# Kernel optimization log

Hardware: AMD Instinct MI355X
Metric: run time of the kernel (lower is better)

## Reference

```python
import jax, jax.numpy as jnp
import numpy as np

S = 2048      # sequence length
E = 2048      # n_embd
H = 16        # n_head
D = E // H    # head_dim = 128
EPS = 1e-5


def _layer_norm(x, w):
    # eqx.nn.LayerNorm, use_bias=False: (x - mean) / sqrt(var + eps) * w
    mu = jnp.mean(x, axis=-1, keepdims=True)
    var = jnp.mean(jnp.square(x - mu), axis=-1, keepdims=True)
    return (x - mu) * jax.lax.rsqrt(var + EPS) * w


def setup_inputs() -> dict:
    key = jax.random.key(0)
    ks = jax.random.split(key, 7)
    x = jax.random.normal(ks[0], (S, E), dtype=jnp.float32)
    # equinox Linear weights are (out_features, in_features); y = W @ x
    w_attn = jax.random.normal(ks[1], (3 * E, E), dtype=jnp.float32) * 0.02
    w_proj_attn = jax.random.normal(ks[2], (E, E), dtype=jnp.float32) * 0.02
    w_fc = jax.random.normal(ks[3], (4 * E, E), dtype=jnp.float32) * 0.02
    w_proj_ffn = jax.random.normal(ks[4], (E, 4 * E), dtype=jnp.float32) * 0.02
    ln1_w = jnp.ones((E,), dtype=jnp.float32)
    ln2_w = jnp.ones((E,), dtype=jnp.float32)
    return {"x": x, "ln1_w": ln1_w, "ln2_w": ln2_w, "w_attn": w_attn,
            "w_proj_attn": w_proj_attn, "w_fc": w_fc, "w_proj_ffn": w_proj_ffn}


def reference(x, ln1_w, ln2_w, w_attn, w_proj_attn, w_fc, w_proj_ffn):
    # --- LN1 + fused QKV projection ---
    h = _layer_norm(x, ln1_w)                       # [S, E]
    qkv = h @ w_attn.T                              # [S, 3E]
    q, k, v = jnp.split(qkv, 3, axis=-1)
    q = q.reshape(S, H, D)
    k = k.reshape(S, H, D)
    v = v.reshape(S, H, D)
    # --- naive causal attention with materialized [H, S, T] scores ---
    scale = 1.0 / jnp.sqrt(jnp.float32(D))
    causal_bias = (jnp.arange(S)[:, None] < jnp.arange(S)[None, :]) * (-10000.0)
    scores = jnp.einsum('shd,thd->hst', q, k) * scale + causal_bias  # [H,S,T]
    probs = jax.nn.softmax(scores, axis=-1)
    attn = jnp.einsum('hst,thd->shd', probs, v).reshape(S, E)
    x = x + attn @ w_proj_attn.T
    # --- LN2 + GELU MLP ---
    h2 = _layer_norm(x, ln2_w)                      # [S, E]
    f = jax.nn.gelu(h2 @ w_fc.T) @ w_proj_ffn.T    # [S,4E] -> [S,E]
    return x + f
```

## Files before the change

kernel.cpp:

```cpp
#include <hip/hip_runtime.h>
#include <hip/hip_bf16.h>

#define S_LEN 2048
#define EMB   2048
#define NH    16
#define HD    128

typedef __bf16 bf16x8 __attribute__((ext_vector_type(8)));
typedef __bf16 bf16x4 __attribute__((ext_vector_type(4)));
typedef float  f32x4  __attribute__((ext_vector_type(4)));
typedef short  s16x4  __attribute__((ext_vector_type(4)));

__device__ __forceinline__ void async_copy16(void* lds, const void* g) {
  __builtin_amdgcn_global_load_lds((__attribute__((address_space(1))) void*)(void*)g,
                                   (__attribute__((address_space(3))) void*)lds, 16, 0, 0);
}

__device__ __forceinline__ unsigned lds_addr(const void* p) {
  return (unsigned)(uintptr_t)(const __attribute__((address_space(3))) char*)p;
}

__device__ __forceinline__ s16x4 tr16(unsigned addr) {
  s16x4 d;
  asm volatile("ds_read_b64_tr_b16 %0, %1" : "=v"(d) : "v"(addr));
  return d;
}

__device__ __forceinline__ float gelu_tanh(float x) {
  float x3 = x * x * x;
  float t  = 0.7978845608028654f * (x + 0.044715f * x3);
  float th = 1.0f - 2.0f / (__expf(2.0f * t) + 1.0f);
  return 0.5f * x * (1.0f + th);
}

__global__ __launch_bounds__(256) void cast_kernel(const float* __restrict__ in,
                                                   __bf16* __restrict__ out, int n) {
  int i = (blockIdx.x * 256 + threadIdx.x) * 4;
  if (i >= n) return;
  float4 v = *(const float4*)(in + i);
  bf16x4 o;
  o[0] = (__bf16)v.x; o[1] = (__bf16)v.y; o[2] = (__bf16)v.z; o[3] = (__bf16)v.w;
  *(bf16x4*)(out + i) = o;
}

__global__ __launch_bounds__(256) void ln_kernel(const float* __restrict__ x,
                                                 const float* __restrict__ w,
                                                 __bf16* __restrict__ out) {
  int row = blockIdx.x;
  int t = threadIdx.x;
  const float* xr = x + (size_t)row * EMB;
  float4 a = *(const float4*)(xr + t * 8);
  float4 b = *(const float4*)(xr + t * 8 + 4);
  float s  = a.x + a.y + a.z + a.w + b.x + b.y + b.z + b.w;
  float sq = a.x*a.x + a.y*a.y + a.z*a.z + a.w*a.w + b.x*b.x + b.y*b.y + b.z*b.z + b.w*b.w;
  #pragma unroll
  for (int o = 32; o > 0; o >>= 1) { s += __shfl_xor(s, o); sq += __shfl_xor(sq, o); }
  __shared__ float red[8];
  if ((t & 63) == 0) { red[t >> 6] = s; red[(t >> 6) + 4] = sq; }
  __syncthreads();
  s  = red[0] + red[1] + red[2] + red[3];
  sq = red[4] + red[5] + red[6] + red[7];
  float mu  = s * (1.0f / EMB);
  float var = sq * (1.0f / EMB) - mu * mu;
  float rs  = rsqrtf(var + 1e-5f);
  float4 w1 = *(const float4*)(w + t * 8);
  float4 w2 = *(const float4*)(w + t * 8 + 4);
  bf16x8 ov;
  ov[0] = (__bf16)((a.x - mu) * rs * w1.x);
  ov[1] = (__bf16)((a.y - mu) * rs * w1.y);
  ov[2] = (__bf16)((a.z - mu) * rs * w1.z);
  ov[3] = (__bf16)((a.w - mu) * rs * w1.w);
  ov[4] = (__bf16)((b.x - mu) * rs * w2.x);
  ov[5] = (__bf16)((b.y - mu) * rs * w2.y);
  ov[6] = (__bf16)((b.z - mu) * rs * w2.z);
  ov[7] = (__bf16)((b.w - mu) * rs * w2.w);
  *(bf16x8*)(out + (size_t)row * EMB + t * 8) = ov;
}

#define MFMA16(AV, BV, MG)                                                                   \
  _Pragma("unroll")                                                                          \
  for (int m = 0; m < 4; m++)                                                                \
    _Pragma("unroll")                                                                        \
    for (int n = 0; n < 4; n++)                                                              \
      acc[(MG) * 4 + m][n] =                                                                 \
          __builtin_amdgcn_mfma_f32_16x16x32_bf16(AV[m], BV[n], acc[(MG) * 4 + m][n], 0, 0, 0);

#define PHASE_TOP()                                                                          \
  __builtin_amdgcn_sched_barrier(0);                                                         \
  __builtin_amdgcn_s_barrier();                                                              \
  asm volatile("s_waitcnt lgkmcnt(0)" ::: "memory");                                         \
  __builtin_amdgcn_sched_barrier(0);                                                         \
  __builtin_amdgcn_s_setprio(1);

#define PHASE_BOT()                                                                          \
  __builtin_amdgcn_s_setprio(0);                                                             \
  __builtin_amdgcn_s_barrier();

template <int EPI>
__global__ __launch_bounds__(512, 2) void gemm256(const __bf16* __restrict__ A,
                                                  const __bf16* __restrict__ B,
                                                  void* __restrict__ Cv,
                                                  int M, int N, int K, int Ksl, int NN) {
  __shared__ __bf16 As[2 * 2 * 256 * 32];
  __shared__ __bf16 Bs[2 * 2 * 256 * 32];

  const int t = threadIdx.x, w = t >> 6, l = t & 63;
  const int fr = l & 15, g = l >> 4;
  const int wr = w >> 2, wc = w & 3;

  const int nwg = gridDim.x;
  const int wg = (blockIdx.x & 7) * (nwg >> 3) + (blockIdx.x >> 3);
  const int NMN = (M >> 8) * NN;
  const int z = wg / NMN, rr = wg - z * NMN;
  const int my = rr / NN, nx = rr - my * NN;
  const int m0 = my * 256, n0 = nx * 256;
  const int kb = z * Ksl;
  const int NT = Ksl >> 6;

  const int srow = t >> 2;
  const int schunk = (t & 3) ^ ((t >> 3) & 3);
  const __bf16* Abase = A + (size_t)(m0 + srow) * K + kb + schunk * 8;
  const __bf16* Bbase = B + (size_t)(n0 + srow) * K + kb + schunk * 8;
  const size_t K128 = (size_t)128 * K;
  __bf16* AsT = &As[t * 8];
  __bf16* BsT = &Bs[t * 8];

  auto stage = [&](const __bf16* base, __bf16* dstT, int kt, int kh) {
    const __bf16* src = base + kt * 64 + kh * 32;
    __bf16* dst = dstT + ((kt & 1) * 2 + kh) * 8192;
    async_copy16(dst, src);
    async_copy16(dst + 4096, src + K128);
  };

  const int gran = (g ^ ((fr >> 1) & 3)) << 3;
  auto rdA = [&](bf16x8* dst, int kt, int kh, int mg) {
    const int ub = ((kt & 1) * 2 + kh) * 256;
    #pragma unroll
    for (int m = 0; m < 4; m++) {
      int row = wr * 128 + (mg * 4 + m) * 16 + fr;
      dst[m] = *(const bf16x8*)&As[(ub + row) * 32 + gran];
    }
  };
  auto rdB = [&](bf16x8* dst, int kt, int kh) {
    const int ub = ((kt & 1) * 2 + kh) * 256;
    #pragma unroll
    for (int n = 0; n < 4; n++) {
      int row = wc * 64 + n * 16 + fr;
      dst[n] = *(const bf16x8*)&Bs[(ub + row) * 32 + gran];
    }
  };

  f32x4 acc[8][4] = {};
  bf16x8 av[4], bX[4], bY[4];

  stage(Abase, AsT, 0, 0); stage(Bbase, BsT, 0, 0);
  stage(Abase, AsT, 0, 1); stage(Bbase, BsT, 0, 1);
  if (NT > 1) { stage(Abase, AsT, 1, 0); stage(Bbase, BsT, 1, 0); }
  asm volatile("s_waitcnt vmcnt(4)" ::: "memory");
  __builtin_amdgcn_s_barrier();

  for (int kt = 0; kt < NT; ++kt) {
    const bool s1 = (kt + 1 < NT), s2 = (kt + 2 < NT);
    rdB(bX, kt, 0);
    rdA(av, kt, 0, 0);
    if (s1) stage(Abase, AsT, kt + 1, 1);
    PHASE_TOP();
    MFMA16(av, bX, 0);
    PHASE_BOT();
    rdA(av, kt, 0, 1);
    if (s1) stage(Bbase, BsT, kt + 1, 1);
    PHASE_TOP();
    MFMA16(av, bX, 1);
    __builtin_amdgcn_s_setprio(0);
    if (s1) { asm volatile("s_waitcnt vmcnt(4)" ::: "memory"); }
    else    { asm volatile("s_waitcnt vmcnt(0)" ::: "memory"); }
    __builtin_amdgcn_s_barrier();
    rdB(bY, kt, 1);
    rdA(av, kt, 1, 0);
    if (s2) stage(Abase, AsT, kt + 2, 0);
    PHASE_TOP();
    MFMA16(av, bY, 0);
    PHASE_BOT();
    rdA(av, kt, 1, 1);
    if (s2) stage(Bbase, BsT, kt + 2, 0);
    PHASE_TOP();
    MFMA16(av, bY, 1);
    PHASE_BOT();
  }

  #pragma unroll
  for (int m = 0; m < 8; m++)
    #pragma unroll
    for (int n = 0; n < 4; n++)
      #pragma unroll
      for (int j = 0; j < 4; j++) {
        int orow = m0 + wr * 128 + m * 16 + g * 4 + j;
        int ocol = n0 + wc * 64 + n * 16 + fr;
        size_t idx = (size_t)orow * N + ocol;
        float v = acc[m][n][j];
        if (EPI == 0) {
          ((__bf16*)Cv)[idx] = (__bf16)v;
        } else if (EPI == 2) {
          ((__bf16*)Cv)[idx] = (__bf16)gelu_tanh(v);
        } else {
          atomicAdd((float*)Cv + idx, v);
        }
      }
}

__global__ __launch_bounds__(256) void attn_kernel(const __bf16* __restrict__ qkv,
                                                   __bf16* __restrict__ out) {
  __shared__ __bf16 Kt[2][64 * 128];
  __shared__ __bf16 Vt[2][64 * 128];
  __shared__ __bf16 Pb[4][16 * 64];

  const int bid = blockIdx.x;
  const int h = bid & 15;
  const int idx = bid >> 4;
  const int qb = (idx < 16) ? idx : 47 - idx;

  const int t = threadIdx.x, w = t >> 6, l = t & 63;
  const int g = l >> 4, fr = l & 15;
  const int fkb = g * 8;
  const int q0 = qb * 64 + w * 16;
  const float scale = 0.08838834764831845f;

  const int krow = w * 4 + g;
  const int kchunk = fr ^ (krow & 7);
  const int vkey = (l >> 1) & 3;
  const int vd0  = (l >> 3) * 16 + (l & 1) * 8;

  const size_t row3E = (size_t)(3 * EMB);
  const __bf16* Kg = qkv + EMB + h * HD;
  const __bf16* Vg = qkv + 2 * EMB + h * HD;

  bf16x8 qf[4];
  #pragma unroll
  for (int kc = 0; kc < 4; kc++)
    qf[kc] = *(const bf16x8*)&qkv[(size_t)(q0 + fr) * row3E + h * HD + kc * 32 + fkb];

  f32x4 o[8] = {};
  float mrun[4] = {-1e30f, -1e30f, -1e30f, -1e30f};
  float lsum[4] = {0.f, 0.f, 0.f, 0.f};

  const unsigned vtrb[2] = { lds_addr(&Vt[0][0]) + g * 2048 + fr * 8,
                             lds_addr(&Vt[1][0]) + g * 2048 + fr * 8 };

  auto stage = [&](int buf, int it) {
    const int t0 = it * 64;
    #pragma unroll
    for (int r = 0; r < 4; r++) {
      async_copy16(&Kt[buf][r * 2048 + w * 512],
                   Kg + (size_t)(t0 + r * 16 + krow) * row3E + kchunk * 8);
      async_copy16(&Vt[buf][(r * 4 + w) * 512],
                   Vg + (size_t)(t0 + r * 16 + w * 4 + vkey) * row3E + vd0);
    }
  };

  const int nt = qb + 1;
  stage(0, 0);
  int cur = 0;

  for (int it = 0; it < nt; it++) {
    __syncthreads();
    if (it + 1 < nt) stage(cur ^ 1, it + 1);
    const int t0 = it * 64;

    f32x4 s[4] = {};
    #pragma unroll
    for (int n = 0; n < 4; n++)
      #pragma unroll
      for (int kc = 0; kc < 4; kc++) {
        bf16x8 kf = *(const bf16x8*)&Kt[cur][(n * 16 + fr) * 128 +
                                            (((kc * 4 + g) ^ (fr & 7)) << 3)];
        s[n] = __builtin_amdgcn_mfma_f32_16x16x32_bf16(qf[kc], kf, s[n], 0, 0, 0);
      }
    #pragma unroll
    for (int n = 0; n < 4; n++)
      #pragma unroll
      for (int j = 0; j < 4; j++) {
        int tcol = t0 + n * 16 + fr;
        int qrow = q0 + g * 4 + j;
        float v = s[n][j] * scale;
        s[n][j] = (tcol > qrow) ? -1e30f : v;
      }
    float pm[4];
    #pragma unroll
    for (int j = 0; j < 4; j++) {
      pm[j] = fmaxf(fmaxf(s[0][j], s[1][j]), fmaxf(s[2][j], s[3][j]));
      #pragma unroll
      for (int off = 1; off < 16; off <<= 1) pm[j] = fmaxf(pm[j], __shfl_xor(pm[j], off));
    }
    float factor[4];
    #pragma unroll
    for (int j = 0; j < 4; j++) {
      float mn = fmaxf(mrun[j], pm[j]);
      factor[j] = __expf(mrun[j] - mn);
      mrun[j] = mn;
    }
    float rs[4] = {0.f, 0.f, 0.f, 0.f};
    #pragma unroll
    for (int n = 0; n < 4; n++)
      #pragma unroll
      for (int j = 0; j < 4; j++) {
        float p = __expf(s[n][j] - mrun[j]);
        s[n][j] = p;
        rs[j] += p;
      }
    #pragma unroll
    for (int j = 0; j < 4; j++) {
      #pragma unroll
      for (int off = 1; off < 16; off <<= 1) rs[j] += __shfl_xor(rs[j], off);
      lsum[j] = lsum[j] * factor[j] + rs[j];
    }
    #pragma unroll
    for (int b = 0; b < 8; b++)
      #pragma unroll
      for (int j = 0; j < 4; j++) o[b][j] *= factor[j];

    #pragma unroll
    for (int n = 0; n < 4; n++)
      #pragma unroll
      for (int j = 0; j < 4; j++) {
        int q   = g * 4 + j;
        int key = n * 16 + fr;
        int cs  = (key >> 3) ^ (q & 7);
        Pb[w][q * 64 + cs * 8 + (key & 7)] = (__bf16)s[n][j];
      }

    bf16x8 pf[2];
    #pragma unroll
    for (int kc = 0; kc < 2; kc++)
      pf[kc] = *(const bf16x8*)&Pb[w][fr * 64 + (((kc * 4 + g) ^ (fr & 7)) << 3)];

    const unsigned vtr = vtrb[cur];
    #pragma unroll
    for (int b = 0; b < 8; b++) {
      s16x4 t00 = tr16(vtr + b * 128);
      s16x4 t01 = tr16(vtr + b * 128 + 1024);
      s16x4 t10 = tr16(vtr + b * 128 + 8192);
      s16x4 t11 = tr16(vtr + b * 128 + 8192 + 1024);
      asm volatile("s_waitcnt lgkmcnt(0)");
      __builtin_amdgcn_sched_barrier(0);
      union { s16x4 hh[2]; bf16x8 v; } u0, u1;
      u0.hh[0] = t00; u0.hh[1] = t01;
      u1.hh[0] = t10; u1.hh[1] = t11;
      o[b] = __builtin_amdgcn_mfma_f32_16x16x32_bf16(pf[0], u0.v, o[b], 0, 0, 0);
      o[b] = __builtin_amdgcn_mfma_f32_16x16x32_bf16(pf[1], u1.v, o[b], 0, 0, 0);
    }
    cur ^= 1;
  }

  float rcp[4];
  #pragma unroll
  for (int j = 0; j < 4; j++) rcp[j] = 1.0f / lsum[j];
  #pragma unroll
  for (int b = 0; b < 8; b++)
    #pragma unroll
    for (int j = 0; j < 4; j++) {
      int qrow = q0 + g * 4 + j;
      out[(size_t)qrow * EMB + h * HD + b * 16 + fr] = (__bf16)(o[b][j] * rcp[j]);
    }
}

extern "C" void kernel_launch(void* const* d_in, const int* in_sizes, int n_in,
                              void* d_out, int out_size, void* d_ws, size_t ws_size,
                              hipStream_t stream) {
  const float* x     = (const float*)d_in[0];
  const float* ln1w  = (const float*)d_in[1];
  const float* ln2w  = (const float*)d_in[2];
  const float* wattn = (const float*)d_in[3];
  const float* wproja= (const float*)d_in[4];
  const float* wfc   = (const float*)d_in[5];
  const float* wprojf= (const float*)d_in[6];
  float* out = (float*)d_out;
  char* ws = (char*)d_ws;

  __bf16* wattn_b  = (__bf16*)(ws);
  __bf16* wproja_b = (__bf16*)(ws + 25165824);
  __bf16* wfc_b    = (__bf16*)(ws + 33554432);
  __bf16* wprojf_b = (__bf16*)(ws + 67108864);
  __bf16* h_b      = (__bf16*)(ws + 100663296);
  __bf16* qkv_b    = (__bf16*)(ws + 109051904);
  __bf16* attn_b   = (__bf16*)(ws + 134217728);
  __bf16* f1_b     = (__bf16*)(ws + 142606336);

  cast_kernel<<<12288, 256, 0, stream>>>(wattn,  wattn_b,  12582912);
  cast_kernel<<<4096,  256, 0, stream>>>(wproja, wproja_b, 4194304);
  cast_kernel<<<16384, 256, 0, stream>>>(wfc,    wfc_b,    16777216);
  cast_kernel<<<16384, 256, 0, stream>>>(wprojf, wprojf_b, 16777216);

  ln_kernel<<<S_LEN, 256, 0, stream>>>(x, ln1w, h_b);
  gemm256<0><<<192, 512, 0, stream>>>(h_b, wattn_b, qkv_b, S_LEN, 3 * EMB, EMB, EMB, 24);
  attn_kernel<<<dim3(512), 256, 0, stream>>>(qkv_b, attn_b);
  (void)hipMemcpyAsync(out, x, (size_t)S_LEN * EMB * sizeof(float), hipMemcpyDeviceToDevice, stream);
  gemm256<4><<<256, 512, 0, stream>>>(attn_b, wproja_b, out, S_LEN, EMB, EMB, EMB / 4, 8);
  ln_kernel<<<S_LEN, 256, 0, stream>>>(out, ln2w, h_b);
  gemm256<2><<<256, 512, 0, stream>>>(h_b, wfc_b, f1_b, S_LEN, 4 * EMB, EMB, EMB, 32);
  gemm256<4><<<256, 512, 0, stream>>>(f1_b, wprojf_b, out, S_LEN, EMB, 4 * EMB, 2048, 8);
}
```

Before: 471.2 us.

## Fuse fp32-to-bf16 weight conversion into GEMM B-operand loading

Drops the four separate weight cast kernels and instead has the GEMM load fp32 weights through registers, convert them to bf16, and write them to LDS in a software-pipelined register-staged path, while A stays on async global-to-LDS copies. This removes a full read and write pass over about 50M weight elements per call. The cost is that the B operand is read as fp32, twice the global traffic per GEMM tile, plus conversion work and register pressure inside the main loop. It also changes the split-K tile mapping so the split index varies fastest, which alters which workgroups share A/B tiles in cache.

```diff
diff --git a/kernel.cpp b/kernel.cpp
--- a/kernel.cpp
+++ b/kernel.cpp
@@ -31,16 +31,6 @@
   float t  = 0.7978845608028654f * (x + 0.044715f * x3);
   float th = 1.0f - 2.0f / (__expf(2.0f * t) + 1.0f);
   return 0.5f * x * (1.0f + th);
-}
-
-__global__ __launch_bounds__(256) void cast_kernel(const float* __restrict__ in,
-                                                   __bf16* __restrict__ out, int n) {
-  int i = (blockIdx.x * 256 + threadIdx.x) * 4;
-  if (i >= n) return;
-  float4 v = *(const float4*)(in + i);
-  bf16x4 o;
-  o[0] = (__bf16)v.x; o[1] = (__bf16)v.y; o[2] = (__bf16)v.z; o[3] = (__bf16)v.w;
-  *(bf16x4*)(out + i) = o;
 }
 
 __global__ __launch_bounds__(256) void ln_kernel(const float* __restrict__ x,
@@ -92,15 +82,12 @@
   __builtin_amdgcn_sched_barrier(0);                                                         \
   __builtin_amdgcn_s_setprio(1);
 
-#define PHASE_BOT()                                                                          \
-  __builtin_amdgcn_s_setprio(0);                                                             \
-  __builtin_amdgcn_s_barrier();
-
 template <int EPI>
 __global__ __launch_bounds__(512, 2) void gemm256(const __bf16* __restrict__ A,
-                                                  const __bf16* __restrict__ B,
+                                                  const float* __restrict__ Bf,
                                                   void* __restrict__ Cv,
-                                                  int M, int N, int K, int Ksl, int NN) {
+                                                  int M, int N, int K, int Ksl,
+                                                  int NN, int NSPLIT) {
   __shared__ __bf16 As[2 * 2 * 256 * 32];
   __shared__ __bf16 Bs[2 * 2 * 256 * 32];
 
@@ -110,9 +97,9 @@
 
   const int nwg = gridDim.x;
   const int wg = (blockIdx.x & 7) * (nwg >> 3) + (blockIdx.x >> 3);
-  const int NMN = (M >> 8) * NN;
-  const int z = wg / NMN, rr = wg - z * NMN;
-  const int my = rr / NN, nx = rr - my * NN;
+  const int z = wg % NSPLIT;
+  const int tile = wg / NSPLIT;
+  const int my = tile / NN, nx = tile - my * NN;
   const int m0 = my * 256, n0 = nx * 256;
   const int kb = z * Ksl;
   const int NT = Ksl >> 6;
@@ -120,16 +107,33 @@
   const int srow = t >> 2;
   const int schunk = (t & 3) ^ ((t >> 3) & 3);
   const __bf16* Abase = A + (size_t)(m0 + srow) * K + kb + schunk * 8;
-  const __bf16* Bbase = B + (size_t)(n0 + srow) * K + kb + schunk * 8;
-  const size_t K128 = (size_t)128 * K;
+  const float*  Bbase = Bf + (size_t)(n0 + srow) * K + kb + schunk * 8;
+  const size_t K128  = (size_t)128 * K;
   __bf16* AsT = &As[t * 8];
   __bf16* BsT = &Bs[t * 8];
 
-  auto stage = [&](const __bf16* base, __bf16* dstT, int kt, int kh) {
-    const __bf16* src = base + kt * 64 + kh * 32;
-    __bf16* dst = dstT + ((kt & 1) * 2 + kh) * 8192;
+  auto stageA = [&](int kt, int kh) {
+    const __bf16* src = Abase + kt * 64 + kh * 32;
+    __bf16* dst = AsT + ((kt & 1) * 2 + kh) * 8192;
     async_copy16(dst, src);
     async_copy16(dst + 4096, src + K128);
+  };
+  auto loadB = [&](float4& x0, float4& x1, float4& x2, float4& x3, int kt, int kh) {
+    const float* s = Bbase + kt * 64 + kh * 32;
+    x0 = *(const float4*)(s);
+    x1 = *(const float4*)(s + 4);
+    x2 = *(const float4*)(s + K128);
+    x3 = *(const float4*)(s + K128 + 4);
+  };
+  auto writeB = [&](float4 x0, float4 x1, float4 x2, float4 x3, int kt, int kh) {
+    __bf16* dst = BsT + ((kt & 1) * 2 + kh) * 8192;
+    bf16x8 v0, v1;
+    v0[0] = (__bf16)x0.x; v0[1] = (__bf16)x0.y; v0[2] = (__bf16)x0.z; v0[3] = (__bf16)x0.w;
+    v0[4] = (__bf16)x1.x; v0[5] = (__bf16)x1.y; v0[6] = (__bf16)x1.z; v0[7] = (__bf16)x1.w;
+    v1[0] = (__bf16)x2.x; v1[1] = (__bf16)x2.y; v1[2] = (__bf16)x2.z; v1[3] = (__bf16)x2.w;
+    v1[4] = (__bf16)x3.x; v1[5] = (__bf16)x3.y; v1[6] = (__bf16)x3.z; v1[7] = (__bf16)x3.w;
+    *(bf16x8*)dst = v0;
+    *(bf16x8*)(dst + 4096) = v1;
   };
 
   const int gran = (g ^ ((fr >> 1) & 3)) << 3;
@@ -152,40 +156,56 @@
 
   f32x4 acc[8][4] = {};
   bf16x8 av[4], bX[4], bY[4];
-
-  stage(Abase, AsT, 0, 0); stage(Bbase, BsT, 0, 0);
-  stage(Abase, AsT, 0, 1); stage(Bbase, BsT, 0, 1);
-  if (NT > 1) { stage(Abase, AsT, 1, 0); stage(Bbase, BsT, 1, 0); }
-  asm volatile("s_waitcnt vmcnt(4)" ::: "memory");
+  float4 s0a, s0b, s0c, s0d;
+  float4 s1a, s1b, s1c, s1d;
+
+  stageA(0, 0); stageA(0, 1);
+  if (NT > 1) stageA(1, 0);
+  {
+    float4 p0, p1, p2, p3;
+    loadB(p0, p1, p2, p3, 0, 0);
+    loadB(s1a, s1b, s1c, s1d, 0, 1);
+    writeB(p0, p1, p2, p3, 0, 0);
+  }
+  asm volatile("s_waitcnt vmcnt(4) lgkmcnt(0)" ::: "memory");
   __builtin_amdgcn_s_barrier();
 
   for (int kt = 0; kt < NT; ++kt) {
     const bool s1 = (kt + 1 < NT), s2 = (kt + 2 < NT);
     rdB(bX, kt, 0);
     rdA(av, kt, 0, 0);
-    if (s1) stage(Abase, AsT, kt + 1, 1);
+    if (s1) stageA(kt + 1, 1);
     PHASE_TOP();
     MFMA16(av, bX, 0);
-    PHASE_BOT();
+    __builtin_amdgcn_s_setprio(0);
+    __builtin_amdgcn_s_barrier();
     rdA(av, kt, 0, 1);
-    if (s1) stage(Bbase, BsT, kt + 1, 1);
+    if (s1) loadB(s0a, s0b, s0c, s0d, kt + 1, 0);
     PHASE_TOP();
     MFMA16(av, bX, 1);
     __builtin_amdgcn_s_setprio(0);
-    if (s1) { asm volatile("s_waitcnt vmcnt(4)" ::: "memory"); }
-    else    { asm volatile("s_waitcnt vmcnt(0)" ::: "memory"); }
+    asm volatile("s_waitcnt vmcnt(6)" ::: "memory");
+    writeB(s1a, s1b, s1c, s1d, kt, 1);
+    asm volatile("s_waitcnt lgkmcnt(0)" ::: "memory");
     __builtin_amdgcn_s_barrier();
     rdB(bY, kt, 1);
     rdA(av, kt, 1, 0);
-    if (s2) stage(Abase, AsT, kt + 2, 0);
+    if (s2) stageA(kt + 2, 0);
     PHASE_TOP();
     MFMA16(av, bY, 0);
-    PHASE_BOT();
+    __builtin_amdgcn_s_setprio(0);
+    __builtin_amdgcn_s_barrier();
     rdA(av, kt, 1, 1);
-    if (s2) stage(Bbase, BsT, kt + 2, 0);
+    if (s1) loadB(s1a, s1b, s1c, s1d, kt + 1, 1);
     PHASE_TOP();
     MFMA16(av, bY, 1);
-    PHASE_BOT();
+    __builtin_amdgcn_s_setprio(0);
+    if (s1) {
+      asm volatile("s_waitcnt vmcnt(6)" ::: "memory");
+      writeB(s0a, s0b, s0c, s0d, kt + 1, 0);
+      asm volatile("s_waitcnt lgkmcnt(0)" ::: "memory");
+    }
+    __builtin_amdgcn_s_barrier();
   }
 
   #pragma unroll
@@ -376,26 +396,17 @@
   float* out = (float*)d_out;
   char* ws = (char*)d_ws;
 
-  __bf16* wattn_b  = (__bf16*)(ws);
-  __bf16* wproja_b = (__bf16*)(ws + 25165824);
-  __bf16* wfc_b    = (__bf16*)(ws + 33554432);
-  __bf16* wprojf_b = (__bf16*)(ws + 67108864);
-  __bf16* h_b      = (__bf16*)(ws + 100663296);
-  __bf16* qkv_b    = (__bf16*)(ws + 109051904);
-  __bf16* attn_b   = (__bf16*)(ws + 134217728);
-  __bf16* f1_b     = (__bf16*)(ws + 142606336);
-
-  cast_kernel<<<12288, 256, 0, stream>>>(wattn,  wattn_b,  12582912);
-  cast_kernel<<<4096,  256, 0, stream>>>(wproja, wproja_b, 4194304);
-  cast_kernel<<<16384, 256, 0, stream>>>(wfc,    wfc_b,    16777216);
-  cast_kernel<<<16384, 256, 0, stream>>>(wprojf, wprojf_b, 16777216);
+  __bf16* h_b    = (__bf16*)(ws + 100663296);
+  __bf16* qkv_b  = (__bf16*)(ws + 109051904);
+  __bf16* attn_b = (__bf16*)(ws + 134217728);
+  __bf16* f1_b   = (__bf16*)(ws + 142606336);
 
   ln_kernel<<<S_LEN, 256, 0, stream>>>(x, ln1w, h_b);
-  gemm256<0><<<192, 512, 0, stream>>>(h_b, wattn_b, qkv_b, S_LEN, 3 * EMB, EMB, EMB, 24);
+  gemm256<0><<<192, 512, 0, stream>>>(h_b, wattn, qkv_b, S_LEN, 3 * EMB, EMB, EMB, 24, 1);
   attn_kernel<<<dim3(512), 256, 0, stream>>>(qkv_b, attn_b);
   (void)hipMemcpyAsync(out, x, (size_t)S_LEN * EMB * sizeof(float), hipMemcpyDeviceToDevice, stream);
-  gemm256<4><<<256, 512, 0, stream>>>(attn_b, wproja_b, out, S_LEN, EMB, EMB, EMB / 4, 8);
+  gemm256<4><<<256, 512, 0, stream>>>(attn_b, wproja, out, S_LEN, EMB, EMB, EMB / 4, 8, 4);
   ln_kernel<<<S_LEN, 256, 0, stream>>>(out, ln2w, h_b);
-  gemm256<2><<<256, 512, 0, stream>>>(h_b, wfc_b, f1_b, S_LEN, 4 * EMB, EMB, EMB, 32);
-  gemm256<4><<<256, 512, 0, stream>>>(f1_b, wprojf_b, out, S_LEN, EMB, 4 * EMB, 2048, 8);
-}
+  gemm256<2><<<256, 512, 0, stream>>>(h_b, wfc, f1_b, S_LEN, 4 * EMB, EMB, EMB, 32, 1);
+  gemm256<4><<<256, 512, 0, stream>>>(f1_b, wprojf, out, S_LEN, EMB, 4 * EMB, 2048, 8, 4);
+}
```

Result: slower. 526.3 us (+11.7%).

## Replace split-K atomics with bf16 partial buffers and fused residual-LN reduction

Applied to the files above, without the earlier changes.

The split-K projection GEMMs now write bf16 partial tiles per K-slice into scratch buffers instead of doing fp32 atomicAdd into the output. The first projection's partials are reduced together with the residual copy inside a new fused LN2 kernel, which also writes the residual stream. The FFN down-projection's partials are summed by a separate add kernel. The split index now varies fastest across workgroups, so the slices of one tile run next to each other. This removes the memcpy and the atomic traffic, at the cost of extra partial reads and writes and bf16 rounding of the partial sums.

```diff
diff --git a/kernel.cpp b/kernel.cpp
--- a/kernel.cpp
+++ b/kernel.cpp
@@ -77,6 +77,65 @@
   *(bf16x8*)(out + (size_t)row * EMB + t * 8) = ov;
 }
 
+__global__ __launch_bounds__(256) void ln_fuse_kernel(const float* __restrict__ x,
+                                                      const __bf16* __restrict__ part,
+                                                      const float* __restrict__ w,
+                                                      __bf16* __restrict__ hout,
+                                                      float* __restrict__ resout) {
+  int row = blockIdx.x;
+  int t = threadIdx.x;
+  const size_t base = (size_t)row * EMB + t * 8;
+  float r[8];
+  {
+    float4 a = *(const float4*)(x + base);
+    float4 b = *(const float4*)(x + base + 4);
+    r[0] = a.x; r[1] = a.y; r[2] = a.z; r[3] = a.w;
+    r[4] = b.x; r[5] = b.y; r[6] = b.z; r[7] = b.w;
+    #pragma unroll
+    for (int z = 0; z < 4; z++) {
+      bf16x8 p = *(const bf16x8*)(part + (size_t)z * S_LEN * EMB + base);
+      #pragma unroll
+      for (int k = 0; k < 8; k++) r[k] += (float)p[k];
+    }
+  }
+  float s = 0.f, sq = 0.f;
+  #pragma unroll
+  for (int k = 0; k < 8; k++) { s += r[k]; sq += r[k] * r[k]; }
+  #pragma unroll
+  for (int o = 32; o > 0; o >>= 1) { s += __shfl_xor(s, o); sq += __shfl_xor(sq, o); }
+  __shared__ float red[8];
+  if ((t & 63) == 0) { red[t >> 6] = s; red[(t >> 6) + 4] = sq; }
+  __syncthreads();
+  s  = red[0] + red[1] + red[2] + red[3];
+  sq = red[4] + red[5] + red[6] + red[7];
+  float mu  = s * (1.0f / EMB);
+  float var = sq * (1.0f / EMB) - mu * mu;
+  float rs  = rsqrtf(var + 1e-5f);
+  float4 w1 = *(const float4*)(w + t * 8);
+  float4 w2 = *(const float4*)(w + t * 8 + 4);
+  float wv[8] = {w1.x, w1.y, w1.z, w1.w, w2.x, w2.y, w2.z, w2.w};
+  bf16x8 ov;
+  #pragma unroll
+  for (int k = 0; k < 8; k++) ov[k] = (__bf16)((r[k] - mu) * rs * wv[k]);
+  *(bf16x8*)(hout + base) = ov;
+  float4 o1 = make_float4(r[0], r[1], r[2], r[3]);
+  float4 o2 = make_float4(r[4], r[5], r[6], r[7]);
+  *(float4*)(resout + base) = o1;
+  *(float4*)(resout + base + 4) = o2;
+}
+
+__global__ __launch_bounds__(256) void add4_kernel(float* __restrict__ out,
+                                                   const __bf16* __restrict__ part) {
+  size_t i = ((size_t)blockIdx.x * 256 + threadIdx.x) * 4;
+  float4 o = *(const float4*)(out + i);
+  #pragma unroll
+  for (int z = 0; z < 4; z++) {
+    bf16x4 p = *(const bf16x4*)(part + (size_t)z * S_LEN * EMB + i);
+    o.x += (float)p[0]; o.y += (float)p[1]; o.z += (float)p[2]; o.w += (float)p[3];
+  }
+  *(float4*)(out + i) = o;
+}
+
 #define MFMA16(AV, BV, MG)                                                                   \
   _Pragma("unroll")                                                                          \
   for (int m = 0; m < 4; m++)                                                                \
@@ -100,7 +159,8 @@
 __global__ __launch_bounds__(512, 2) void gemm256(const __bf16* __restrict__ A,
                                                   const __bf16* __restrict__ B,
                                                   void* __restrict__ Cv,
-                                                  int M, int N, int K, int Ksl, int NN) {
+                                                  int M, int N, int K, int Ksl,
+                                                  int NN, int NSPLIT) {
   __shared__ __bf16 As[2 * 2 * 256 * 32];
   __shared__ __bf16 Bs[2 * 2 * 256 * 32];
 
@@ -110,9 +170,9 @@
 
   const int nwg = gridDim.x;
   const int wg = (blockIdx.x & 7) * (nwg >> 3) + (blockIdx.x >> 3);
-  const int NMN = (M >> 8) * NN;
-  const int z = wg / NMN, rr = wg - z * NMN;
-  const int my = rr / NN, nx = rr - my * NN;
+  const int z = wg % NSPLIT;
+  const int tile = wg / NSPLIT;
+  const int my = tile / NN, nx = tile - my * NN;
   const int m0 = my * 256, n0 = nx * 256;
   const int kb = z * Ksl;
   const int NT = Ksl >> 6;
@@ -188,6 +248,7 @@
     PHASE_BOT();
   }
 
+  const size_t zoff = (size_t)z * M * N;
   #pragma unroll
   for (int m = 0; m < 8; m++)
     #pragma unroll
@@ -203,7 +264,7 @@
         } else if (EPI == 2) {
           ((__bf16*)Cv)[idx] = (__bf16)gelu_tanh(v);
         } else {
-          atomicAdd((float*)Cv + idx, v);
+          ((__bf16*)Cv)[zoff + idx] = (__bf16)v;
         }
       }
 }
@@ -384,6 +445,8 @@
   __bf16* qkv_b    = (__bf16*)(ws + 109051904);
   __bf16* attn_b   = (__bf16*)(ws + 134217728);
   __bf16* f1_b     = (__bf16*)(ws + 142606336);
+  __bf16* p1_part  = f1_b;
+  __bf16* p2_part  = qkv_b;
 
   cast_kernel<<<12288, 256, 0, stream>>>(wattn,  wattn_b,  12582912);
   cast_kernel<<<4096,  256, 0, stream>>>(wproja, wproja_b, 4194304);
@@ -391,11 +454,11 @@
   cast_kernel<<<16384, 256, 0, stream>>>(wprojf, wprojf_b, 16777216);
 
   ln_kernel<<<S_LEN, 256, 0, stream>>>(x, ln1w, h_b);
-  gemm256<0><<<192, 512, 0, stream>>>(h_b, wattn_b, qkv_b, S_LEN, 3 * EMB, EMB, EMB, 24);
+  gemm256<0><<<192, 512, 0, stream>>>(h_b, wattn_b, qkv_b, S_LEN, 3 * EMB, EMB, EMB, 24, 1);
   attn_kernel<<<dim3(512), 256, 0, stream>>>(qkv_b, attn_b);
-  (void)hipMemcpyAsync(out, x, (size_t)S_LEN * EMB * sizeof(float), hipMemcpyDeviceToDevice, stream);
-  gemm256<4><<<256, 512, 0, stream>>>(attn_b, wproja_b, out, S_LEN, EMB, EMB, EMB / 4, 8);
-  ln_kernel<<<S_LEN, 256, 0, stream>>>(out, ln2w, h_b);
-  gemm256<2><<<256, 512, 0, stream>>>(h_b, wfc_b, f1_b, S_LEN, 4 * EMB, EMB, EMB, 32);
-  gemm256<4><<<256, 512, 0, stream>>>(f1_b, wprojf_b, out, S_LEN, EMB, 4 * EMB, 2048, 8);
-}
+  gemm256<5><<<256, 512, 0, stream>>>(attn_b, wproja_b, p1_part, S_LEN, EMB, EMB, EMB / 4, 8, 4);
+  ln_fuse_kernel<<<S_LEN, 256, 0, stream>>>(x, p1_part, ln2w, h_b, out);
+  gemm256<2><<<256, 512, 0, stream>>>(h_b, wfc_b, f1_b, S_LEN, 4 * EMB, EMB, EMB, 32, 1);
+  gemm256<5><<<256, 512, 0, stream>>>(f1_b, wprojf_b, p2_part, S_LEN, EMB, 4 * EMB, 2048, 8, 4);
+  add4_kernel<<<4096, 256, 0, stream>>>(out, p2_part);
+}
```

Measured after the change: 406.1 us. 13.8% less time.
